# Kernel tuning notes

Hardware: AMD Instinct MI355X
Metric: run time of the kernel (lower is better)

Reference implementation:

```python
import jax, jax.numpy as jnp
import numpy as np

N, D, H, DH, DFF, E = 4096, 512, 8, 64, 2048, 65536


def setup_inputs() -> dict:
    key = jax.random.key(0)
    ks = jax.random.split(key, 20)
    g = lambda k, s: jax.random.normal(k, s, dtype=jnp.float32) * 0.02
    inp = {
        'x': jax.random.normal(ks[0], (N, D), dtype=jnp.float32),
        'edge_index': jax.random.randint(ks[1], (2, E), 0, N),
        'edge_attr': jax.random.uniform(ks[2], (E,), dtype=jnp.float32),
        'Wg': g(ks[3], (D, D)), 'bg': jnp.zeros((D,), jnp.float32),
        'ln1_s': jnp.ones((D,), jnp.float32), 'ln1_b': jnp.zeros((D,), jnp.float32),
        'Wq': g(ks[4], (D, D)), 'bq': jnp.zeros((D,), jnp.float32),
        'Wk': g(ks[5], (D, D)), 'bk': jnp.zeros((D,), jnp.float32),
        'Wv': g(ks[6], (D, D)), 'bv': jnp.zeros((D,), jnp.float32),
        'Wo': g(ks[7], (D, D)), 'bo': jnp.zeros((D,), jnp.float32),
        'ln2_s': jnp.ones((D,), jnp.float32), 'ln2_b': jnp.zeros((D,), jnp.float32),
        'W1': g(ks[8], (D, DFF)), 'b1': jnp.zeros((DFF,), jnp.float32),
        'W2': g(ks[9], (DFF, D)), 'b2': jnp.zeros((D,), jnp.float32),
        'Wa': g(ks[10], (2 * D, D)), 'ba': jnp.zeros((D,), jnp.float32),
    }
    return inp


def _ln(x, s, b):
    m = x.mean(-1, keepdims=True)
    v = ((x - m) ** 2).mean(-1, keepdims=True)
    return (x - m) * jax.lax.rsqrt(v + 1e-5) * s + b


def _gcn(x, edge_index, ew, Wg, bg):
    # GCNConv: linear, add self-loops (weight 1), sym deg normalization, scatter-add
    xt = x @ Wg                                   # [N, D]
    src = jnp.concatenate([edge_index[0], jnp.arange(N)])
    dst = jnp.concatenate([edge_index[1], jnp.arange(N)])
    w = jnp.concatenate([ew, jnp.ones((N,), ew.dtype)])
    deg = jax.ops.segment_sum(w, dst, num_segments=N)
    dinv = jnp.where(deg > 0, jax.lax.rsqrt(jnp.maximum(deg, 1e-12)), 0.0)
    coef = dinv[src] * w * dinv[dst]              # [E+N]
    out = jax.ops.segment_sum(xt[src] * coef[:, None], dst, num_segments=N)
    return out + bg


def _tfm(x, p):
    # pre-LN vanilla transformer block over all N nodes as one sequence
    h = _ln(x, p['ln1_s'], p['ln1_b'])
    q = (h @ p['Wq'] + p['bq']).reshape(N, H, DH)
    k = (h @ p['Wk'] + p['bk']).reshape(N, H, DH)
    v = (h @ p['Wv'] + p['bv']).reshape(N, H, DH)
    scores = jnp.einsum('nhd,mhd->hnm', q, k) / np.sqrt(DH)
    a = jax.nn.softmax(scores, axis=-1)
    o = jnp.einsum('hnm,mhd->nhd', a, v).reshape(N, D)
    x = x + o @ p['Wo'] + p['bo']
    h2 = _ln(x, p['ln2_s'], p['ln2_b'])
    mlp = jax.nn.gelu(h2 @ p['W1'] + p['b1']) @ p['W2'] + p['b2']
    return x + mlp


def reference(x, edge_index, edge_attr, Wg, bg, ln1_s, ln1_b, Wq, bq, Wk, bk, Wv, bv,
              Wo, bo, ln2_s, ln2_b, W1, b1, W2, b2, Wa, ba):
    p = dict(ln1_s=ln1_s, ln1_b=ln1_b, Wq=Wq, bq=bq, Wk=Wk, bk=bk, Wv=Wv, bv=bv,
             Wo=Wo, bo=bo, ln2_s=ln2_s, ln2_b=ln2_b, W1=W1, b1=b1, W2=W2, b2=b2)
    mp = _gcn(x, edge_index, edge_attr, Wg, bg)
    tf = _tfm(x, p)
    return x + jnp.concatenate([mp, tf], axis=-1) @ Wa + ba
```

## Files before the change

### kernel.cpp

```cpp
#include <hip/hip_runtime.h>
#include <math.h>

#define N_NODES 4096
#define DMODEL  512
#define NHEAD   8
#define DHEAD   64
#define DFF     2048
#define NEDGE   65536
#define QKVLD   1536

typedef unsigned short u16;
typedef __bf16 bf16x8 __attribute__((ext_vector_type(8)));
typedef float  f32x4  __attribute__((ext_vector_type(4)));
typedef short  s16x4  __attribute__((ext_vector_type(4)));

#if defined(__has_builtin)
#if __has_builtin(__builtin_amdgcn_mfma_f32_16x16x16bf16_1k)
#define HAS_MFMA_1K 1
#endif
#endif

__device__ inline f32x4 mfma16(bf16x8 a, bf16x8 b, f32x4 c) {
    return __builtin_amdgcn_mfma_f32_16x16x32_bf16(a, b, c, 0, 0, 0);
}

#ifdef HAS_MFMA_1K
__device__ inline f32x4 mfma1k(s16x4 a, s16x4 b, f32x4 c) {
    return __builtin_amdgcn_mfma_f32_16x16x16bf16_1k(a, b, c, 0, 0, 0);
}
__device__ inline s16x4 pack_bf4(f32x4 p) {
    union { float f; unsigned u; } a0, a1, a2, a3;
    a0.f = p[0]; a1.f = p[1]; a2.f = p[2]; a3.f = p[3];
    unsigned lo = __builtin_amdgcn_perm(a1.u + 0x8000u, a0.u + 0x8000u, 0x07060302u);
    unsigned hi = __builtin_amdgcn_perm(a3.u + 0x8000u, a2.u + 0x8000u, 0x07060302u);
    union { unsigned u[2]; s16x4 v; } r;
    r.u[0] = lo; r.u[1] = hi;
    return r.v;
}
#endif

__device__ inline u16 f2bf(float f) {
    union { float f; unsigned u; } v; v.f = f;
    unsigned r = v.u + 0x7fff + ((v.u >> 16) & 1);
    return (u16)(r >> 16);
}

__device__ inline float bf2f(u16 v) {
    union { unsigned u; float f; } t; t.u = ((unsigned)v) << 16; return t.f;
}

__device__ inline float gelu_tanh(float x) {
    float x3 = x * x * x;
    float t = tanhf(0.7978845608028654f * (x + 0.044715f * x3));
    return 0.5f * x * (1.0f + t);
}

#define GBM 128
#define GBN 128
#define GBK 32
#define GP  40

template <int ACT, int OBF16>
__launch_bounds__(256)
__global__ void mfma_gemm(const u16* __restrict__ A, const u16* __restrict__ Bt,
                          const float* __restrict__ bias, const float* __restrict__ res,
                          void* __restrict__ Cout, int M, int Nn, int K, float scale,
                          int ldC, int ldRes) {
    __shared__ u16 Asm[2][GBM * GP];
    __shared__ u16 Bsm[2][GBN * GP];

    const int tid = threadIdx.x;
    const int w = tid >> 6;
    const int lane = tid & 63;
    const int quad = lane >> 4;
    const int l15 = lane & 15;
    const int row0 = blockIdx.y * GBM;
    const int col0 = blockIdx.x * GBN;
    const int wm = (w & 1) * 64;
    const int wn = (w >> 1) * 64;

    f32x4 acc[4][4];
#pragma unroll
    for (int i = 0; i < 4; ++i)
#pragma unroll
        for (int j = 0; j < 4; ++j) acc[i][j] = (f32x4){0.f, 0.f, 0.f, 0.f};

    const int c1 = tid, c2 = tid + 256;
    const int ar1 = c1 >> 2, ak1 = (c1 & 3) * 8;
    const int ar2 = c2 >> 2, ak2 = (c2 & 3) * 8;

    {
        uint4 a0 = *(const uint4*)&A [(size_t)(row0 + ar1) * K + ak1];
        uint4 a1 = *(const uint4*)&A [(size_t)(row0 + ar2) * K + ak2];
        uint4 b0 = *(const uint4*)&Bt[(size_t)(col0 + ar1) * K + ak1];
        uint4 b1 = *(const uint4*)&Bt[(size_t)(col0 + ar2) * K + ak2];
        *(uint4*)&Asm[0][ar1 * GP + ak1] = a0;
        *(uint4*)&Asm[0][ar2 * GP + ak2] = a1;
        *(uint4*)&Bsm[0][ar1 * GP + ak1] = b0;
        *(uint4*)&Bsm[0][ar2 * GP + ak2] = b1;
    }
    __syncthreads();

    const int nT = K / GBK;
    for (int t = 0; t < nT; ++t) {
        const int buf = t & 1;
        uint4 an0, an1, bn0, bn1;
        if (t + 1 < nT) {
            const int k0 = (t + 1) * GBK;
            an0 = *(const uint4*)&A [(size_t)(row0 + ar1) * K + k0 + ak1];
            an1 = *(const uint4*)&A [(size_t)(row0 + ar2) * K + k0 + ak2];
            bn0 = *(const uint4*)&Bt[(size_t)(col0 + ar1) * K + k0 + ak1];
            bn1 = *(const uint4*)&Bt[(size_t)(col0 + ar2) * K + k0 + ak2];
        }
        bf16x8 af[4], bf[4];
#pragma unroll
        for (int i = 0; i < 4; ++i) {
            af[i] = *(const bf16x8*)&Asm[buf][(wm + i * 16 + l15) * GP + quad * 8];
            bf[i] = *(const bf16x8*)&Bsm[buf][(wn + i * 16 + l15) * GP + quad * 8];
        }
#pragma unroll
        for (int i = 0; i < 4; ++i)
#pragma unroll
            for (int j = 0; j < 4; ++j)
                acc[i][j] = mfma16(af[i], bf[j], acc[i][j]);
        if (t + 1 < nT) {
            *(uint4*)&Asm[buf ^ 1][ar1 * GP + ak1] = an0;
            *(uint4*)&Asm[buf ^ 1][ar2 * GP + ak2] = an1;
            *(uint4*)&Bsm[buf ^ 1][ar1 * GP + ak1] = bn0;
            *(uint4*)&Bsm[buf ^ 1][ar2 * GP + ak2] = bn1;
            __syncthreads();
        }
    }

#pragma unroll
    for (int j = 0; j < 4; ++j) {
        const int col = col0 + wn + j * 16 + l15;
        const float bc = bias ? bias[col] : 0.f;
#pragma unroll
        for (int i = 0; i < 4; ++i) {
#pragma unroll
            for (int r = 0; r < 4; ++r) {
                const int row = row0 + wm + i * 16 + quad * 4 + r;
                float o = (acc[i][j][r] + bc) * scale;
                if (ACT == 1) o = gelu_tanh(o);
                if (res) o += res[(size_t)row * ldRes + col];
                if (OBF16)
                    ((u16*)Cout)[(size_t)row * ldC + col] = f2bf(o);
                else
                    ((float*)Cout)[(size_t)row * ldC + col] = o;
            }
        }
    }
}

template <int ACT, int OBF16>
__launch_bounds__(512)
__global__ void mfma_gemm64(const u16* __restrict__ A, const u16* __restrict__ Bt,
                            const float* __restrict__ bias, const float* __restrict__ res,
                            void* __restrict__ Cout, int M, int Nn, int K, float scale,
                            int ldC, int ldRes) {
    __shared__ u16 Asm[2][64 * GP];
    __shared__ u16 Bsm[2][128 * GP];

    const int tid = threadIdx.x;
    const int w = tid >> 6;
    const int lane = tid & 63;
    const int quad = lane >> 4;
    const int l15 = lane & 15;
    const int row0 = blockIdx.y * 64;
    const int col0 = blockIdx.x * GBN;
    const int rh = (w & 1) * 32;
    const int cg = (w >> 1) * 32;

    f32x4 acc[2][2];
#pragma unroll
    for (int i = 0; i < 2; ++i)
#pragma unroll
        for (int j = 0; j < 2; ++j) acc[i][j] = (f32x4){0.f, 0.f, 0.f, 0.f};

    const int brow = tid >> 2, bk = (tid & 3) * 8;
    const int arow = (tid & 255) >> 2, ak = (tid & 3) * 8;
    const bool doA = (tid < 256);

    {
        uint4 b0 = *(const uint4*)&Bt[(size_t)(col0 + brow) * K + bk];
        *(uint4*)&Bsm[0][brow * GP + bk] = b0;
        if (doA) {
            uint4 a0 = *(const uint4*)&A[(size_t)(row0 + arow) * K + ak];
            *(uint4*)&Asm[0][arow * GP + ak] = a0;
        }
    }
    __syncthreads();

    const int nT = K / GBK;
    for (int t = 0; t < nT; ++t) {
        const int buf = t & 1;
        uint4 an, bn;
        if (t + 1 < nT) {
            const int k0 = (t + 1) * GBK;
            bn = *(const uint4*)&Bt[(size_t)(col0 + brow) * K + k0 + bk];
            if (doA) an = *(const uint4*)&A[(size_t)(row0 + arow) * K + k0 + ak];
        }
        bf16x8 af[2], bf[2];
#pragma unroll
        for (int i = 0; i < 2; ++i)
            af[i] = *(const bf16x8*)&Asm[buf][(rh + i * 16 + l15) * GP + quad * 8];
#pragma unroll
        for (int j = 0; j < 2; ++j)
            bf[j] = *(const bf16x8*)&Bsm[buf][(cg + j * 16 + l15) * GP + quad * 8];
#pragma unroll
        for (int i = 0; i < 2; ++i)
#pragma unroll
            for (int j = 0; j < 2; ++j)
                acc[i][j] = mfma16(af[i], bf[j], acc[i][j]);
        if (t + 1 < nT) {
            *(uint4*)&Bsm[buf ^ 1][brow * GP + bk] = bn;
            if (doA) *(uint4*)&Asm[buf ^ 1][arow * GP + ak] = an;
            __syncthreads();
        }
    }

#pragma unroll
    for (int j = 0; j < 2; ++j) {
        const int col = col0 + cg + j * 16 + l15;
        const float bc = bias ? bias[col] : 0.f;
#pragma unroll
        for (int i = 0; i < 2; ++i) {
#pragma unroll
            for (int r = 0; r < 4; ++r) {
                const int row = row0 + rh + i * 16 + quad * 4 + r;
                float o = (acc[i][j][r] + bc) * scale;
                if (ACT == 1) o = gelu_tanh(o);
                if (res) o += res[(size_t)row * ldRes + col];
                if (OBF16)
                    ((u16*)Cout)[(size_t)row * ldC + col] = f2bf(o);
                else
                    ((float*)Cout)[(size_t)row * ldC + col] = o;
            }
        }
    }
}

__launch_bounds__(256)
__global__ void qkvg_gemm(const u16* __restrict__ xb, const u16* __restrict__ hb,
                          const u16* __restrict__ Wall,
                          const float* __restrict__ bq, const float* __restrict__ bk,
                          const float* __restrict__ bv,
                          u16* __restrict__ xtb, u16* __restrict__ qkvb,
                          u16* __restrict__ vtb) {
    __shared__ u16 Asm[2][64 * GP];
    __shared__ u16 Bsm[2][128 * GP];

    const int tid = threadIdx.x;
    const int w = tid >> 6;
    const int lane = tid & 63;
    const int quad = lane >> 4;
    const int l15 = lane & 15;
    const int row0 = blockIdx.y * 64;
    const int col0 = blockIdx.x * GBN;
    const int wn = w * 32;
    const int K = DMODEL;
    const u16* A = (col0 < 512) ? xb : hb;

    f32x4 acc[4][2];
#pragma unroll
    for (int i = 0; i < 4; ++i)
#pragma unroll
        for (int j = 0; j < 2; ++j) acc[i][j] = (f32x4){0.f, 0.f, 0.f, 0.f};

    const int c1 = tid, c2 = tid + 256;
    const int ar1 = c1 >> 2, ak1 = (c1 & 3) * 8;
    const int ar2 = c2 >> 2, ak2 = (c2 & 3) * 8;

    {
        uint4 a0 = *(const uint4*)&A   [(size_t)(row0 + ar1) * K + ak1];
        uint4 b0 = *(const uint4*)&Wall[(size_t)(col0 + ar1) * K + ak1];
        uint4 b1 = *(const uint4*)&Wall[(size_t)(col0 + ar2) * K + ak2];
        *(uint4*)&Asm[0][ar1 * GP + ak1] = a0;
        *(uint4*)&Bsm[0][ar1 * GP + ak1] = b0;
        *(uint4*)&Bsm[0][ar2 * GP + ak2] = b1;
    }
    __syncthreads();

    const int nT = K / GBK;
    for (int t = 0; t < nT; ++t) {
        const int buf = t & 1;
        uint4 an, bn0, bn1;
        if (t + 1 < nT) {
            const int k0 = (t + 1) * GBK;
            an  = *(const uint4*)&A   [(size_t)(row0 + ar1) * K + k0 + ak1];
            bn0 = *(const uint4*)&Wall[(size_t)(col0 + ar1) * K + k0 + ak1];
            bn1 = *(const uint4*)&Wall[(size_t)(col0 + ar2) * K + k0 + ak2];
        }
        bf16x8 af[4], bf[2];
#pragma unroll
        for (int i = 0; i < 4; ++i)
            af[i] = *(const bf16x8*)&Asm[buf][(i * 16 + l15) * GP + quad * 8];
#pragma unroll
        for (int j = 0; j < 2; ++j)
            bf[j] = *(const bf16x8*)&Bsm[buf][(wn + j * 16 + l15) * GP + quad * 8];
#pragma unroll
        for (int i = 0; i < 4; ++i)
#pragma unroll
            for (int j = 0; j < 2; ++j)
                acc[i][j] = mfma16(af[i], bf[j], acc[i][j]);
        if (t + 1 < nT) {
            *(uint4*)&Asm[buf ^ 1][ar1 * GP + ak1] = an;
            *(uint4*)&Bsm[buf ^ 1][ar1 * GP + ak1] = bn0;
            *(uint4*)&Bsm[buf ^ 1][ar2 * GP + ak2] = bn1;
            __syncthreads();
        }
    }

#pragma unroll
    for (int j = 0; j < 2; ++j) {
        const int col = col0 + wn + j * 16 + l15;
        if (col < 512) {
#pragma unroll
            for (int i = 0; i < 4; ++i)
#pragma unroll
                for (int r = 0; r < 4; ++r)
                    xtb[(size_t)(row0 + i * 16 + quad * 4 + r) * 512 + col] =
                        f2bf(acc[i][j][r]);
        } else if (col < 1536) {
            const float bc = (col < 1024) ? bq[col - 512] : bk[col - 1024];
            const float scale = (col < 1024) ? 0.125f : 1.0f;
#pragma unroll
            for (int i = 0; i < 4; ++i)
#pragma unroll
                for (int r = 0; r < 4; ++r)
                    qkvb[(size_t)(row0 + i * 16 + quad * 4 + r) * QKVLD + col - 512] =
                        f2bf((acc[i][j][r] + bc) * scale);
        } else {
            const int hd = col - 1536;
            const float bc = bv[hd];
#pragma unroll
            for (int i = 0; i < 4; ++i) {
                ushort4 pk;
                pk.x = f2bf(acc[i][j][0] + bc);
                pk.y = f2bf(acc[i][j][1] + bc);
                pk.z = f2bf(acc[i][j][2] + bc);
                pk.w = f2bf(acc[i][j][3] + bc);
                *(uint2*)&vtb[(size_t)hd * N_NODES + row0 + i * 16 + quad * 4] =
                    *(uint2*)&pk;
            }
        }
    }
}

__device__ inline float block_sum_256(float v, float* red4) {
#pragma unroll
    for (int o = 32; o > 0; o >>= 1) v += __shfl_down(v, o, 64);
    const int lane = threadIdx.x & 63;
    const int w = threadIdx.x >> 6;
    if (lane == 0) red4[w] = v;
    __syncthreads();
    return red4[0] + red4[1] + red4[2] + red4[3];
}

__launch_bounds__(256)
__global__ void prep_kernel(
    const float* __restrict__ Wg, const float* __restrict__ Wq,
    const float* __restrict__ Wk, const float* __restrict__ Wv,
    const float* __restrict__ Wo, const float* __restrict__ W1,
    const float* __restrict__ W2, const float* __restrict__ Wa,
    u16* __restrict__ Wgt, u16* __restrict__ Wqt, u16* __restrict__ Wkt,
    u16* __restrict__ Wvt, u16* __restrict__ Wot, u16* __restrict__ W1t,
    u16* __restrict__ W2t, u16* __restrict__ Wat,
    const float* __restrict__ x, u16* __restrict__ xb,
    const float* __restrict__ ln1s, const float* __restrict__ ln1b,
    u16* __restrict__ hb, float* __restrict__ deg, int* __restrict__ cnt) {
    __shared__ u16 t[32][34];
    __shared__ float redA[4];
    __shared__ float redB[4];
    const int id = blockIdx.x;

    if (id < 3840) {
        const float* W; u16* Wt; int K, Nn, bx, by;
        if (id < 1280) {
            const int m = id >> 8, tt = id & 255;
            bx = tt & 15; by = tt >> 4; K = 512; Nn = 512;
            W  = (m == 0) ? Wg  : (m == 1) ? Wq  : (m == 2) ? Wk  : (m == 3) ? Wv  : Wo;
            Wt = (m == 0) ? Wgt : (m == 1) ? Wqt : (m == 2) ? Wkt : (m == 3) ? Wvt : Wot;
        } else if (id < 2304) {
            const int tt = id - 1280; bx = tt & 63; by = tt >> 6;
            K = 512; Nn = 2048; W = W1; Wt = W1t;
        } else if (id < 3328) {
            const int tt = id - 2304; bx = tt & 15; by = tt >> 4;
            K = 2048; Nn = 512; W = W2; Wt = W2t;
        } else {
            const int tt = id - 3328; bx = tt & 15; by = tt >> 4;
            K = 1024; Nn = 512; W = Wa; Wt = Wat;
        }
        const int k0 = by * 32, n0 = bx * 32;
        const int r = threadIdx.x >> 3, c4 = (threadIdx.x & 7) * 4;
        float4 v = *(const float4*)&W[(size_t)(k0 + r) * Nn + n0 + c4];
        t[r][c4 + 0] = f2bf(v.x); t[r][c4 + 1] = f2bf(v.y);
        t[r][c4 + 2] = f2bf(v.z); t[r][c4 + 3] = f2bf(v.w);
        __syncthreads();
        u16 tmp[4];
#pragma unroll
        for (int i = 0; i < 4; ++i) tmp[i] = t[c4 + i][r];
        u16* op = Wt + (size_t)(n0 + r) * K + k0 + c4;
        *(uint2*)op = *(uint2*)tmp;
    } else if (id < 5888) {
        size_t i = ((size_t)(id - 3840) * 256 + threadIdx.x) * 4;
        float4 v = *(const float4*)&x[i];
        ushort4 o;
        o.x = f2bf(v.x); o.y = f2bf(v.y); o.z = f2bf(v.z); o.w = f2bf(v.w);
        *(ushort4*)&xb[i] = o;
    } else if (id < 9984) {
        const int row = id - 5888;
        const int tid = threadIdx.x;
        const float* xr = x + (size_t)row * DMODEL;
        float v0 = xr[tid], v1 = xr[tid + 256];
        float total = block_sum_256(v0 + v1, redA);
        float mean = total * (1.0f / DMODEL);
        float d0 = v0 - mean, d1 = v1 - mean;
        float sq = block_sum_256(d0 * d0 + d1 * d1, redB);
        float inv = rsqrtf(sq * (1.0f / DMODEL) + 1e-5f);
        hb[(size_t)row * DMODEL + tid] = f2bf(d0 * inv * ln1s[tid] + ln1b[tid]);
        hb[(size_t)row * DMODEL + tid + 256] =
            f2bf(d1 * inv * ln1s[tid + 256] + ln1b[tid + 256]);
    } else {
        int i = (id - 9984) * 256 + threadIdx.x;
        deg[i] = 1.0f;
        cnt[i] = 0;
    }
}

__launch_bounds__(256)
__global__ void ln_kernel(const float* __restrict__ X, const float* __restrict__ s,
                          const float* __restrict__ b, u16* __restrict__ Y) {
    __shared__ float redA[4];
    __shared__ float redB[4];
    const int row = blockIdx.x;
    const int tid = threadIdx.x;
    const float* xr = X + (size_t)row * DMODEL;
    float v0 = xr[tid], v1 = xr[tid + 256];
    float total = block_sum_256(v0 + v1, redA);
    float mean = total * (1.0f / DMODEL);
    float d0 = v0 - mean, d1 = v1 - mean;
    float sq = block_sum_256(d0 * d0 + d1 * d1, redB);
    float inv = rsqrtf(sq * (1.0f / DMODEL) + 1e-5f);
    Y[(size_t)row * DMODEL + tid] = f2bf(d0 * inv * s[tid] + b[tid]);
    Y[(size_t)row * DMODEL + tid + 256] = f2bf(d1 * inv * s[tid + 256] + b[tid + 256]);
}

__global__ void gcn_count_kernel(const int* __restrict__ ei, const float* __restrict__ ew,
                                 float* __restrict__ deg, int* __restrict__ cnt) {
    int e = blockIdx.x * 256 + threadIdx.x;
    int d = ei[NEDGE + e];
    atomicAdd(&cnt[d], 1);
    atomicAdd(&deg[d], ew[e]);
}

__launch_bounds__(256)
__global__ void gcn_prefix_kernel(const int* __restrict__ cnt, int* __restrict__ off,
                                  int* __restrict__ cur, const float* __restrict__ deg,
                                  float* __restrict__ dinv) {
    __shared__ int part[256];
    const int tid = threadIdx.x;
    int local[16];
    int s = 0;
#pragma unroll
    for (int i = 0; i < 16; ++i) { local[i] = s; s += cnt[tid * 16 + i]; }
    part[tid] = s;
#pragma unroll
    for (int i = 0; i < 16; ++i) {
        const int n = tid * 16 + i;
        float d = deg[n];
        dinv[n] = (d > 0.f) ? rsqrtf(fmaxf(d, 1e-12f)) : 0.f;
    }
    __syncthreads();
    if (tid == 0) {
        int run = 0;
        for (int j = 0; j < 256; ++j) { int t = part[j]; part[j] = run; run += t; }
        off[N_NODES] = run;
    }
    __syncthreads();
    int p = part[tid];
#pragma unroll
    for (int i = 0; i < 16; ++i) {
        off[tid * 16 + i] = p + local[i];
        cur[tid * 16 + i] = p + local[i];
    }
}

__global__ void gcn_fill_kernel(const int* __restrict__ ei, const float* __restrict__ ew,
                                int* __restrict__ cur, int* __restrict__ esrc,
                                float* __restrict__ eww) {
    int e = blockIdx.x * 256 + threadIdx.x;
    int s = ei[e], d = ei[NEDGE + e];
    int pos = atomicAdd(&cur[d], 1);
    esrc[pos] = s;
    eww[pos] = ew[e];
}

__launch_bounds__(256)
__global__ void gcn_gather_kernel(const u16* __restrict__ xtb, const int* __restrict__ off,
                                  const int* __restrict__ esrc, const float* __restrict__ eww,
                                  const float* __restrict__ dinv, const float* __restrict__ bg,
                                  u16* __restrict__ catb) {
    const int d = blockIdx.x;
    const int b0 = off[d], b1 = off[d + 1];
    const float did = dinv[d];
    const int c = threadIdx.x * 2;
    float a0 = 0.f, a1 = 0.f;
    for (int j = b0; j < b1; ++j) {
        const int s = esrc[j];
        const float coef = dinv[s] * eww[j] * did;
        const unsigned pv = *(const unsigned*)&xtb[(size_t)s * DMODEL + c];
        a0 += coef * bf2f((u16)(pv & 0xffff));
        a1 += coef * bf2f((u16)(pv >> 16));
    }
    {
        const unsigned pv = *(const unsigned*)&xtb[(size_t)d * DMODEL + c];
        const float sl = did * did;
        a0 += sl * bf2f((u16)(pv & 0xffff));
        a1 += sl * bf2f((u16)(pv >> 16));
    }
    const unsigned pk = (unsigned)f2bf(a0 + bg[c]) | ((unsigned)f2bf(a1 + bg[c + 1]) << 16);
    *(unsigned*)&catb[(size_t)d * 1024 + c] = pk;
}

#define TK 64
#define AP 88
#define NSPLIT 4
#define KSPAN (N_NODES / NSPLIT)

__launch_bounds__(128)
__global__ void attn_kernel(const u16* __restrict__ Qkv, const u16* __restrict__ Vtb,
                            float* __restrict__ Op0, float* __restrict__ Op1,
                            float* __restrict__ Op2, float* __restrict__ Op3,
                            float* __restrict__ lpart) {
    __shared__ u16 Ks[64 * AP];
    __shared__ u16 Vs[64 * AP];
#ifndef HAS_MFMA_1K
    __shared__ u16 Ps[2][2][16 * AP];
#endif

    const int h = blockIdx.x;
    const int q0 = blockIdx.y * 64;
    const int sp = blockIdx.z;
    float* __restrict__ Opx = (sp == 0) ? Op0 : (sp == 1) ? Op1 : (sp == 2) ? Op2 : Op3;
    const int kbase = sp * KSPAN;

    const int tid = threadIdx.x;
    const int w = tid >> 6;
    const int lane = tid & 63;
    const int quad = lane >> 4;
    const int l15 = lane & 15;

    const u16* qp = Qkv + (size_t)(q0 + w * 32 + l15) * QKVLD + h * DHEAD + quad * 8;
    bf16x8 qf[2][2];
    qf[0][0] = *(const bf16x8*)qp;
    qf[0][1] = *(const bf16x8*)(qp + 32);
    qf[1][0] = *(const bf16x8*)(qp + 16 * QKVLD);
    qf[1][1] = *(const bf16x8*)(qp + 16 * QKVLD + 32);

    f32x4 Oa[2][4];
#pragma unroll
    for (int a = 0; a < 2; ++a)
#pragma unroll
        for (int g = 0; g < 4; ++g) Oa[a][g] = (f32x4){0.f, 0.f, 0.f, 0.f};
    float ls[2] = {0.f, 0.f};

    const int sr = tid >> 1, sc = (tid & 1) * 32;

    for (int kt = kbase; kt < kbase + KSPAN; kt += TK) {
        {
            const uint4* kg = (const uint4*)(Qkv + (size_t)(kt + sr) * QKVLD + 512 + h * DHEAD + sc);
            uint4* kd = (uint4*)&Ks[sr * AP + sc];
            kd[0] = kg[0]; kd[1] = kg[1]; kd[2] = kg[2]; kd[3] = kg[3];
            const uint4* vg = (const uint4*)(Vtb + ((size_t)h * DHEAD + sr) * N_NODES + kt + sc);
            uint4* vd = (uint4*)&Vs[sr * AP + sc];
            vd[0] = vg[0]; vd[1] = vg[1]; vd[2] = vg[2]; vd[3] = vg[3];
        }
        __syncthreads();

        f32x4 St[2][4];
#pragma unroll
        for (int f = 0; f < 4; ++f) {
            const u16* kr = &Ks[(f * 16 + l15) * AP + quad * 8];
            bf16x8 k0 = *(const bf16x8*)kr;
            bf16x8 k1 = *(const bf16x8*)(kr + 32);
#pragma unroll
            for (int a = 0; a < 2; ++a) {
                f32x4 z = (f32x4){0.f, 0.f, 0.f, 0.f};
                z = mfma16(k0, qf[a][0], z);
                St[a][f] = mfma16(k1, qf[a][1], z);
            }
        }

#ifdef HAS_MFMA_1K
        s16x4 pk[2][4];
#pragma unroll
        for (int a = 0; a < 2; ++a)
#pragma unroll
            for (int f = 0; f < 4; ++f) {
                f32x4 p;
                p[0] = __expf(St[a][f][0]);
                p[1] = __expf(St[a][f][1]);
                p[2] = __expf(St[a][f][2]);
                p[3] = __expf(St[a][f][3]);
                ls[a] += (p[0] + p[1]) + (p[2] + p[3]);
                pk[a][f] = pack_bf4(p);
            }
#pragma unroll
        for (int f = 0; f < 4; ++f)
#pragma unroll
            for (int g = 0; g < 4; ++g) {
                const s16x4 vv = *(const s16x4*)&Vs[(g * 16 + l15) * AP + f * 16 + quad * 4];
                Oa[0][g] = mfma1k(pk[0][f], vv, Oa[0][g]);
                Oa[1][g] = mfma1k(pk[1][f], vv, Oa[1][g]);
            }
#else
        bf16x8 pa[2][2];
#pragma unroll
        for (int a = 0; a < 2; ++a) {
            u16* pw = Ps[w][a];
#pragma unroll
            for (int f = 0; f < 4; ++f) {
                float p0 = __expf(St[a][f][0]);
                float p1 = __expf(St[a][f][1]);
                float p2 = __expf(St[a][f][2]);
                float p3 = __expf(St[a][f][3]);
                ls[a] += (p0 + p1) + (p2 + p3);
                ushort4 pkk;
                pkk.x = f2bf(p0); pkk.y = f2bf(p1); pkk.z = f2bf(p2); pkk.w = f2bf(p3);
                *(uint2*)&pw[l15 * AP + f * 16 + quad * 4] = *(uint2*)&pkk;
            }
            const u16* pr = &pw[l15 * AP + quad * 8];
            pa[a][0] = *(const bf16x8*)pr;
            pa[a][1] = *(const bf16x8*)(pr + 32);
        }
#pragma unroll
        for (int g = 0; g < 4; ++g) {
            const u16* vr = &Vs[(g * 16 + l15) * AP + quad * 8];
            bf16x8 v0 = *(const bf16x8*)vr;
            bf16x8 v1 = *(const bf16x8*)(vr + 32);
#pragma unroll
            for (int a = 0; a < 2; ++a) {
                Oa[a][g] = mfma16(pa[a][0], v0, Oa[a][g]);
                Oa[a][g] = mfma16(pa[a][1], v1, Oa[a][g]);
            }
        }
#endif
        __syncthreads();
    }

#pragma unroll
    for (int a = 0; a < 2; ++a) {
        float s = ls[a];
        s += __shfl_xor(s, 16, 64);
        s += __shfl_xor(s, 32, 64);
        const int rowbase = q0 + w * 32 + a * 16;
        if (quad == 0)
            lpart[(size_t)(sp * NHEAD + h) * N_NODES + rowbase + l15] = s;
#pragma unroll
        for (int r = 0; r < 4; ++r) {
            float* op = Opx + (size_t)(rowbase + quad * 4 + r) * DMODEL + h * DHEAD + l15;
#pragma unroll
            for (int g = 0; g < 4; ++g) op[g * 16] = Oa[a][g][r];
        }
    }
}

__global__ void attn_reduce_kernel(const float* __restrict__ Op0, const float* __restrict__ Op1,
                                   const float* __restrict__ Op2, const float* __restrict__ Op3,
                                   const float* __restrict__ lpart, u16* __restrict__ attb) {
    size_t i4 = ((size_t)blockIdx.x * 256 + threadIdx.x) * 4;
    const int row = (int)(i4 >> 9);
    const int h = ((int)i4 & 511) >> 6;
    float4 o0 = *(const float4*)&Op0[i4];
    float4 o1 = *(const float4*)&Op1[i4];
    float4 o2 = *(const float4*)&Op2[i4];
    float4 o3 = *(const float4*)&Op3[i4];
    const float* lp = lpart + (size_t)h * N_NODES + row;
    const size_t S = (size_t)NHEAD * N_NODES;
    float inv = 1.0f / (lp[0] + lp[S] + lp[2 * S] + lp[3 * S]);
    ushort4 r;
    r.x = f2bf((o0.x + o1.x + o2.x + o3.x) * inv);
    r.y = f2bf((o0.y + o1.y + o2.y + o3.y) * inv);
    r.z = f2bf((o0.z + o1.z + o2.z + o3.z) * inv);
    r.w = f2bf((o0.w + o1.w + o2.w + o3.w) * inv);
    *(ushort4*)&attb[i4] = r;
}

static void mgemm(hipStream_t st, const u16* A, const u16* Bt, const float* bias,
                  const float* res, void* C, int M, int Nn, int K, float scale,
                  int act, int obf16, int ldC, int ldRes) {
    dim3 g(Nn / GBN, M / GBM), b(256);
    if (act)
        hipLaunchKernelGGL((mfma_gemm<1, 1>), g, b, 0, st, A, Bt, bias, res, C, M, Nn, K, scale, ldC, ldRes);
    else if (obf16)
        hipLaunchKernelGGL((mfma_gemm<0, 1>), g, b, 0, st, A, Bt, bias, res, C, M, Nn, K, scale, ldC, ldRes);
    else
        hipLaunchKernelGGL((mfma_gemm<0, 0>), g, b, 0, st, A, Bt, bias, res, C, M, Nn, K, scale, ldC, ldRes);
}

static void mgemm64(hipStream_t st, const u16* A, const u16* Bt, const float* bias,
                    const float* res, void* C, int M, int Nn, int K, float scale,
                    int act, int obf16, int ldC, int ldRes) {
    dim3 g(Nn / GBN, M / 64), b(512);
    if (act)
        hipLaunchKernelGGL((mfma_gemm64<1, 1>), g, b, 0, st, A, Bt, bias, res, C, M, Nn, K, scale, ldC, ldRes);
    else if (obf16)
        hipLaunchKernelGGL((mfma_gemm64<0, 1>), g, b, 0, st, A, Bt, bias, res, C, M, Nn, K, scale, ldC, ldRes);
    else
        hipLaunchKernelGGL((mfma_gemm64<0, 0>), g, b, 0, st, A, Bt, bias, res, C, M, Nn, K, scale, ldC, ldRes);
}

extern "C" void kernel_launch(void* const* d_in, const int* in_sizes, int n_in,
                              void* d_out, int out_size, void* d_ws, size_t ws_size,
                              hipStream_t stream) {
    const float* x    = (const float*)d_in[0];
    const int*   ei   = (const int*)d_in[1];
    const float* ew   = (const float*)d_in[2];
    const float* Wg   = (const float*)d_in[3];
    const float* bg   = (const float*)d_in[4];
    const float* ln1s = (const float*)d_in[5];
    const float* ln1b = (const float*)d_in[6];
    const float* Wq   = (const float*)d_in[7];
    const float* bq   = (const float*)d_in[8];
    const float* Wk   = (const float*)d_in[9];
    const float* bk   = (const float*)d_in[10];
    const float* Wv   = (const float*)d_in[11];
    const float* bv   = (const float*)d_in[12];
    const float* Wo   = (const float*)d_in[13];
    const float* bo   = (const float*)d_in[14];
    const float* ln2s = (const float*)d_in[15];
    const float* ln2b = (const float*)d_in[16];
    const float* W1   = (const float*)d_in[17];
    const float* b1   = (const float*)d_in[18];
    const float* W2   = (const float*)d_in[19];
    const float* b2   = (const float*)d_in[20];
    const float* Wa   = (const float*)d_in[21];
    const float* ba   = (const float*)d_in[22];
    float* out = (float*)d_out;
    float* ws  = (float*)d_ws;

    const size_t SLOT = (size_t)N_NODES * DMODEL;

    u16*   xtb = (u16*)ws;
    float* Op2 = ws;
    float* x1  = ws;
    float* lpart = ws + SLOT;
    int*   esrc  = (int*)(ws + SLOT + 262144);
    float* eww   = (float*)(esrc + NEDGE);
    int*   off   = (int*)(eww + NEDGE);
    int*   cur   = off + 4100;
    int*   cnt   = cur + 4096;
    float* Op3 = ws + 2 * SLOT;
    u16* hb   = (u16*)(ws + 3 * SLOT);
    u16* attb = hb + SLOT;
    u16* h2b  = hb + SLOT;
    u16* qkvb = (u16*)(ws + 4 * SLOT);
    u16* vtb  = (u16*)(ws + 5 * SLOT) + SLOT;
    float* Op0  = ws + 6 * SLOT;
    float* Op1  = ws + 7 * SLOT;
    u16*   midb = (u16*)(ws + 6 * SLOT);
    u16* catb = (u16*)(ws + 8 * SLOT);
    u16* xb   = catb;
    u16* Wgt = (u16*)(ws + 9 * SLOT);
    u16* Wqt = Wgt + 262144;
    u16* Wkt = Wqt + 262144;
    u16* Wvt = Wkt + 262144;
    u16* Wot = Wvt + 262144;
    u16* W1t = Wot + 262144;
    u16* W2t = W1t + 1048576;
    u16* Wat = W2t + 1048576;
    float* deg  = (float*)(Wat + 524288);
    float* dinv = deg + N_NODES;

    hipLaunchKernelGGL(prep_kernel, dim3(10000), dim3(256), 0, stream,
                       Wg, Wq, Wk, Wv, Wo, W1, W2, Wa,
                       Wgt, Wqt, Wkt, Wvt, Wot, W1t, W2t, Wat,
                       x, xb, ln1s, ln1b, hb, deg, cnt);

    hipLaunchKernelGGL(qkvg_gemm, dim3(16, 64), dim3(256), 0, stream,
                       xb, hb, Wgt, bq, bk, bv, xtb, qkvb, vtb);

    hipLaunchKernelGGL(gcn_count_kernel, dim3(NEDGE / 256), dim3(256), 0, stream, ei, ew, deg, cnt);
    hipLaunchKernelGGL(gcn_prefix_kernel, dim3(1), dim3(256), 0, stream, cnt, off, cur, deg, dinv);
    hipLaunchKernelGGL(gcn_fill_kernel, dim3(NEDGE / 256), dim3(256), 0, stream, ei, ew, cur, esrc, eww);
    hipLaunchKernelGGL(gcn_gather_kernel, dim3(N_NODES), dim3(256), 0, stream,
                       xtb, off, esrc, eww, dinv, bg, catb);

    hipLaunchKernelGGL(attn_kernel, dim3(NHEAD, N_NODES / 64, NSPLIT), dim3(128), 0, stream,
                       qkvb, vtb, Op0, Op1, Op2, Op3, lpart);
    hipLaunchKernelGGL(attn_reduce_kernel, dim3((int)(SLOT / 1024)), dim3(256), 0, stream,
                       Op0, Op1, Op2, Op3, lpart, attb);

    mgemm64(stream, attb, Wot, bo, x, x1, N_NODES, DMODEL, DMODEL, 1.0f, 0, 0, DMODEL, DMODEL);
    hipLaunchKernelGGL(ln_kernel, dim3(N_NODES), dim3(256), 0, stream, x1, ln2s, ln2b, h2b);
    mgemm(stream, h2b, W1t, b1, nullptr, midb, N_NODES, DFF, DMODEL, 1.0f, 1, 1, DFF, DFF);
    mgemm64(stream, midb, W2t, b2, x1, catb + 512, N_NODES, DMODEL, DFF, 1.0f, 0, 1, 1024, DMODEL);

    mgemm64(stream, catb, Wat, ba, x, out, N_NODES, DMODEL, 2 * DMODEL, 1.0f, 0, 0, DMODEL, DMODEL);
}
```

Before: 360.0 us.

## Widen attention blocks to 128 queries and route the FFN up-projection through gemm64

The attention kernel now runs 256 threads (4 waves) per block covering 128 queries instead of 64. Each K/V tile loaded into shared memory is therefore reused by twice as many queries, halving K/V global traffic per query. K and V loading is split between the two thread halves, and the shared-memory row padding shrinks from 88 to 72, which may change bank-conflict behaviour. The W1 GEMM now uses the 64-row gemm64 kernel instead of the removed 128x128 kernel, which gives more blocks but less reuse per block.

```diff
diff --git a/kernel.cpp b/kernel.cpp
--- a/kernel.cpp
+++ b/kernel.cpp
@@ -55,103 +55,9 @@
     return 0.5f * x * (1.0f + t);
 }
 
-#define GBM 128
 #define GBN 128
 #define GBK 32
 #define GP  40
-
-template <int ACT, int OBF16>
-__launch_bounds__(256)
-__global__ void mfma_gemm(const u16* __restrict__ A, const u16* __restrict__ Bt,
-                          const float* __restrict__ bias, const float* __restrict__ res,
-                          void* __restrict__ Cout, int M, int Nn, int K, float scale,
-                          int ldC, int ldRes) {
-    __shared__ u16 Asm[2][GBM * GP];
-    __shared__ u16 Bsm[2][GBN * GP];
-
-    const int tid = threadIdx.x;
-    const int w = tid >> 6;
-    const int lane = tid & 63;
-    const int quad = lane >> 4;
-    const int l15 = lane & 15;
-    const int row0 = blockIdx.y * GBM;
-    const int col0 = blockIdx.x * GBN;
-    const int wm = (w & 1) * 64;
-    const int wn = (w >> 1) * 64;
-
-    f32x4 acc[4][4];
-#pragma unroll
-    for (int i = 0; i < 4; ++i)
-#pragma unroll
-        for (int j = 0; j < 4; ++j) acc[i][j] = (f32x4){0.f, 0.f, 0.f, 0.f};
-
-    const int c1 = tid, c2 = tid + 256;
-    const int ar1 = c1 >> 2, ak1 = (c1 & 3) * 8;
-    const int ar2 = c2 >> 2, ak2 = (c2 & 3) * 8;
-
-    {
-        uint4 a0 = *(const uint4*)&A [(size_t)(row0 + ar1) * K + ak1];
-        uint4 a1 = *(const uint4*)&A [(size_t)(row0 + ar2) * K + ak2];
-        uint4 b0 = *(const uint4*)&Bt[(size_t)(col0 + ar1) * K + ak1];
-        uint4 b1 = *(const uint4*)&Bt[(size_t)(col0 + ar2) * K + ak2];
-        *(uint4*)&Asm[0][ar1 * GP + ak1] = a0;
-        *(uint4*)&Asm[0][ar2 * GP + ak2] = a1;
-        *(uint4*)&Bsm[0][ar1 * GP + ak1] = b0;
-        *(uint4*)&Bsm[0][ar2 * GP + ak2] = b1;
-    }
-    __syncthreads();
-
-    const int nT = K / GBK;
-    for (int t = 0; t < nT; ++t) {
-        const int buf = t & 1;
-        uint4 an0, an1, bn0, bn1;
-        if (t + 1 < nT) {
-            const int k0 = (t + 1) * GBK;
-            an0 = *(const uint4*)&A [(size_t)(row0 + ar1) * K + k0 + ak1];
-            an1 = *(const uint4*)&A [(size_t)(row0 + ar2) * K + k0 + ak2];
-            bn0 = *(const uint4*)&Bt[(size_t)(col0 + ar1) * K + k0 + ak1];
-            bn1 = *(const uint4*)&Bt[(size_t)(col0 + ar2) * K + k0 + ak2];
-        }
-        bf16x8 af[4], bf[4];
-#pragma unroll
-        for (int i = 0; i < 4; ++i) {
-            af[i] = *(const bf16x8*)&Asm[buf][(wm + i * 16 + l15) * GP + quad * 8];
-            bf[i] = *(const bf16x8*)&Bsm[buf][(wn + i * 16 + l15) * GP + quad * 8];
-        }
-#pragma unroll
-        for (int i = 0; i < 4; ++i)
-#pragma unroll
-            for (int j = 0; j < 4; ++j)
-                acc[i][j] = mfma16(af[i], bf[j], acc[i][j]);
-        if (t + 1 < nT) {
-            *(uint4*)&Asm[buf ^ 1][ar1 * GP + ak1] = an0;
-            *(uint4*)&Asm[buf ^ 1][ar2 * GP + ak2] = an1;
-            *(uint4*)&Bsm[buf ^ 1][ar1 * GP + ak1] = bn0;
-            *(uint4*)&Bsm[buf ^ 1][ar2 * GP + ak2] = bn1;
-            __syncthreads();
-        }
-    }
-
-#pragma unroll
-    for (int j = 0; j < 4; ++j) {
-        const int col = col0 + wn + j * 16 + l15;
-        const float bc = bias ? bias[col] : 0.f;
-#pragma unroll
-        for (int i = 0; i < 4; ++i) {
-#pragma unroll
-            for (int r = 0; r < 4; ++r) {
-                const int row = row0 + wm + i * 16 + quad * 4 + r;
-                float o = (acc[i][j][r] + bc) * scale;
-                if (ACT == 1) o = gelu_tanh(o);
-                if (res) o += res[(size_t)row * ldRes + col];
-                if (OBF16)
-                    ((u16*)Cout)[(size_t)row * ldC + col] = f2bf(o);
-                else
-                    ((float*)Cout)[(size_t)row * ldC + col] = o;
-            }
-        }
-    }
-}
 
 template <int ACT, int OBF16>
 __launch_bounds__(512)
@@ -525,11 +431,11 @@
 }
 
 #define TK 64
-#define AP 88
+#define AP 72
 #define NSPLIT 4
 #define KSPAN (N_NODES / NSPLIT)
 
-__launch_bounds__(128)
+__launch_bounds__(256)
 __global__ void attn_kernel(const u16* __restrict__ Qkv, const u16* __restrict__ Vtb,
                             float* __restrict__ Op0, float* __restrict__ Op1,
                             float* __restrict__ Op2, float* __restrict__ Op3,
@@ -537,11 +443,11 @@
     __shared__ u16 Ks[64 * AP];
     __shared__ u16 Vs[64 * AP];
 #ifndef HAS_MFMA_1K
-    __shared__ u16 Ps[2][2][16 * AP];
+    __shared__ u16 Ps[4][2][16 * AP];
 #endif
 
     const int h = blockIdx.x;
-    const int q0 = blockIdx.y * 64;
+    const int q0 = blockIdx.y * 128;
     const int sp = blockIdx.z;
     float* __restrict__ Opx = (sp == 0) ? Op0 : (sp == 1) ? Op1 : (sp == 2) ? Op2 : Op3;
     const int kbase = sp * KSPAN;
@@ -566,15 +472,17 @@
         for (int g = 0; g < 4; ++g) Oa[a][g] = (f32x4){0.f, 0.f, 0.f, 0.f};
     float ls[2] = {0.f, 0.f};
 
-    const int sr = tid >> 1, sc = (tid & 1) * 32;
+    const int srow = (tid & 127) >> 1;
+    const int scol = (tid & 1) * 32;
 
     for (int kt = kbase; kt < kbase + KSPAN; kt += TK) {
-        {
-            const uint4* kg = (const uint4*)(Qkv + (size_t)(kt + sr) * QKVLD + 512 + h * DHEAD + sc);
-            uint4* kd = (uint4*)&Ks[sr * AP + sc];
+        if (tid < 128) {
+            const uint4* kg = (const uint4*)(Qkv + (size_t)(kt + srow) * QKVLD + 512 + h * DHEAD + scol);
+            uint4* kd = (uint4*)&Ks[srow * AP + scol];
             kd[0] = kg[0]; kd[1] = kg[1]; kd[2] = kg[2]; kd[3] = kg[3];
-            const uint4* vg = (const uint4*)(Vtb + ((size_t)h * DHEAD + sr) * N_NODES + kt + sc);
-            uint4* vd = (uint4*)&Vs[sr * AP + sc];
+        } else {
+            const uint4* vg = (const uint4*)(Vtb + ((size_t)h * DHEAD + srow) * N_NODES + kt + scol);
+            uint4* vd = (uint4*)&Vs[srow * AP + scol];
             vd[0] = vg[0]; vd[1] = vg[1]; vd[2] = vg[2]; vd[3] = vg[3];
         }
         __syncthreads();
@@ -686,18 +594,6 @@
     r.z = f2bf((o0.z + o1.z + o2.z + o3.z) * inv);
     r.w = f2bf((o0.w + o1.w + o2.w + o3.w) * inv);
     *(ushort4*)&attb[i4] = r;
-}
-
-static void mgemm(hipStream_t st, const u16* A, const u16* Bt, const float* bias,
-                  const float* res, void* C, int M, int Nn, int K, float scale,
-                  int act, int obf16, int ldC, int ldRes) {
-    dim3 g(Nn / GBN, M / GBM), b(256);
-    if (act)
-        hipLaunchKernelGGL((mfma_gemm<1, 1>), g, b, 0, st, A, Bt, bias, res, C, M, Nn, K, scale, ldC, ldRes);
-    else if (obf16)
-        hipLaunchKernelGGL((mfma_gemm<0, 1>), g, b, 0, st, A, Bt, bias, res, C, M, Nn, K, scale, ldC, ldRes);
-    else
-        hipLaunchKernelGGL((mfma_gemm<0, 0>), g, b, 0, st, A, Bt, bias, res, C, M, Nn, K, scale, ldC, ldRes);
 }
 
 static void mgemm64(hipStream_t st, const u16* A, const u16* Bt, const float* bias,
@@ -788,14 +684,14 @@
     hipLaunchKernelGGL(gcn_gather_kernel, dim3(N_NODES), dim3(256), 0, stream,
                        xtb, off, esrc, eww, dinv, bg, catb);
 
-    hipLaunchKernelGGL(attn_kernel, dim3(NHEAD, N_NODES / 64, NSPLIT), dim3(128), 0, stream,
+    hipLaunchKernelGGL(attn_kernel, dim3(NHEAD, N_NODES / 128, NSPLIT), dim3(256), 0, stream,
                        qkvb, vtb, Op0, Op1, Op2, Op3, lpart);
     hipLaunchKernelGGL(attn_reduce_kernel, dim3((int)(SLOT / 1024)), dim3(256), 0, stream,
                        Op0, Op1, Op2, Op3, lpart, attb);
 
     mgemm64(stream, attb, Wot, bo, x, x1, N_NODES, DMODEL, DMODEL, 1.0f, 0, 0, DMODEL, DMODEL);
     hipLaunchKernelGGL(ln_kernel, dim3(N_NODES), dim3(256), 0, stream, x1, ln2s, ln2b, h2b);
-    mgemm(stream, h2b, W1t, b1, nullptr, midb, N_NODES, DFF, DMODEL, 1.0f, 1, 1, DFF, DFF);
+    mgemm64(stream, h2b, W1t, b1, nullptr, midb, N_NODES, DFF, DMODEL, 1.0f, 1, 1, DFF, DFF);
     mgemm64(stream, midb, W2t, b2, x1, catb + 512, N_NODES, DMODEL, DFF, 1.0f, 0, 1, 1024, DMODEL);
 
     mgemm64(stream, catb, Wat, ba, x, out, N_NODES, DMODEL, 2 * DMODEL, 1.0f, 0, 0, DMODEL, DMODEL);
```

Result: faster. 340.7 us (-5.3%).
